# Kernel optimization log

Hardware: AMD Instinct MI355X
Metric: run time of the kernel (lower is better)

The kernel has to match this reference:

```python
import jax, jax.numpy as jnp
import numpy as np

LOW_THRESH, HIGH_THRESH = 0.1, 0.2   # kornia canny defaults
HYST_ITERS = 10                      # fixed-point hysteresis iterations (fixed for jit)


def _gaussian_kernel5(sigma=1.0):
    x = jnp.arange(5, dtype=jnp.float32) - 2.0
    g = jnp.exp(-0.5 * (x / sigma) ** 2)
    g = g / g.sum()
    return jnp.outer(g, g)  # [5,5]


def _conv2d(x, k):
    # x: [B,1,H,W]; k: [kh,kw]; reflect pad + VALID conv == SAME with reflect border
    kh, kw = k.shape
    xp = jnp.pad(x, ((0, 0), (0, 0), (kh // 2, kh // 2), (kw // 2, kw // 2)), mode="reflect")
    return jax.lax.conv_general_dilated(
        xp, k[None, None], (1, 1), "VALID",
        dimension_numbers=("NCHW", "OIHW", "NCHW"))


def _shift(x, dy, dx):
    # value of neighbor at (i+dy, j+dx), zero-padded border; x: [B,1,H,W]
    H, W = x.shape[2], x.shape[3]
    xp = jnp.pad(x, ((0, 0), (0, 0), (1, 1), (1, 1)))
    return xp[:, :, 1 + dy:1 + dy + H, 1 + dx:1 + dx + W]


def _canny_edges(img):
    # img: [B,3,H,W] in [0,1] -> binary edge map [B,1,H,W]
    gray = 0.299 * img[:, :1] + 0.587 * img[:, 1:2] + 0.114 * img[:, 2:3]
    blur = _conv2d(gray, _gaussian_kernel5())
    sobel_x = jnp.array([[-1., 0., 1.], [-2., 0., 2.], [-1., 0., 1.]], jnp.float32)
    gx = _conv2d(blur, sobel_x)
    gy = _conv2d(blur, sobel_x.T)
    mag = jnp.sqrt(gx * gx + gy * gy + 1e-12)
    ang = jnp.arctan2(gy, gx)

    # non-maximum suppression: quantize gradient direction to 4 bins (0/45/90/135 deg)
    b = jnp.mod(jnp.round(ang / (jnp.pi / 4.0)), 4).astype(jnp.int32)  # [B,1,H,W]
    n_pos = jnp.stack([_shift(mag, 0, 1), _shift(mag, 1, 1),
                       _shift(mag, 1, 0), _shift(mag, 1, -1)], axis=0)  # [4,B,1,H,W]
    n_neg = jnp.stack([_shift(mag, 0, -1), _shift(mag, -1, -1),
                       _shift(mag, -1, 0), _shift(mag, -1, 1)], axis=0)
    n1 = jnp.take_along_axis(n_pos, b[None], axis=0)[0]
    n2 = jnp.take_along_axis(n_neg, b[None], axis=0)[0]
    nms = jnp.where((mag >= n1) & (mag >= n2), mag, 0.0)

    # double threshold: strong=1.0, weak=0.5
    edges = jnp.where(nms >= HIGH_THRESH, 1.0,
                      jnp.where(nms >= LOW_THRESH, 0.5, 0.0))

    # hysteresis: weak pixels with a strong 8-neighbor become strong (iterated)
    def body(_, e):
        strong = (e == 1.0).astype(e.dtype)
        nb = jax.lax.reduce_window(strong, 0.0, jax.lax.max,
                                   (1, 1, 3, 3), (1, 1, 1, 1), "SAME")
        promoted = (e == 0.5) & (nb > 0.5)
        return jnp.where(promoted, 1.0, e)

    edges = jax.lax.fori_loop(0, HYST_ITERS, body, edges)
    return (edges == 1.0).astype(jnp.float32)


def setup_inputs() -> dict:
    key = jax.random.key(0)
    k1, k2 = jax.random.split(key)
    shape = (16, 3, 512, 512)
    return {"y_hat": jax.random.uniform(k1, shape, jnp.float32),
            "y": jax.random.uniform(k2, shape, jnp.float32)}


def reference(y_hat, y):
    y_hat_edges = _canny_edges(y_hat)
    y_edges = _canny_edges(y)
    return jnp.mean(jnp.abs(y_hat_edges - y_edges))  # F.l1_loss, mean reduction
```

## Files before the change

kernel.cpp:

```cpp
#include <hip/hip_runtime.h>
#include <math.h>

#define H 512
#define W 512
#define IMG (H*W)
#define NIMG 32
#define NSTRIP 10
#define SW 56
#define RB 32
#define NBAND 16
#define NHYST_BLK 1024

typedef unsigned long long u64;

__device__ __forceinline__ int reflect_idx(int i, int n) {
    if (i < 0) i = -i;
    if (i >= n) i = 2 * n - 2 - i;
    return i;
}

__device__ __forceinline__ float bperm_f(int addr, float v) {
    return __int_as_float(__builtin_amdgcn_ds_bpermute(addr, __float_as_int(v)));
}

#define S0c 0.05448868454964294f
#define S1c 0.35317871110251920f
#define S2c 0.94551131545035710f
#define S3c 1.29364257779496160f
#define A1c 0.05448868454964294f
#define A2c 0.24420134200323332f
#define A3c 0.34813126234460456f

__global__ __launch_bounds__(256, 5) void k_edges(const float* __restrict__ yhat,
                                                  const float* __restrict__ yy,
                                                  u64* __restrict__ strongP,
                                                  u64* __restrict__ weakP,
                                                  unsigned int* __restrict__ counters) {
    const int wid = blockIdx.x * 4 + (threadIdx.x >> 6);
    const int lane = threadIdx.x & 63;

    if (wid == 0 && lane == 0) { counters[0] = 0u; counters[1] = 0u; }

    const int n = wid / (NSTRIP * NBAND);
    const int rem = wid - n * (NSTRIP * NBAND);
    const int s = rem / NBAND;
    const int band = rem - s * NBAND;
    const int y0 = band * RB;
    const float* src = (n < 16) ? (yhat + (size_t)n * 3 * IMG)
                                : (yy + (size_t)(n - 16) * 3 * IMG);
    const float* __restrict__ srcR = src;
    const float* __restrict__ srcG = src + IMG;
    const float* __restrict__ srcB = src + 2 * IMG;

    const int c = s * SW - 4 + lane;
    const int cx = reflect_idx(c, W);
    const bool colok = ((unsigned)c < (unsigned)W);
    const u64 omask = (s == 9) ? 0xFFull : 0x00FFFFFFFFFFFFFFull;

    const int aM1 = ((lane - 1) << 2), aP1 = ((lane + 1) << 2);
    const int aM2 = ((lane - 2) << 2), aP2 = ((lane + 2) << 2);
    const int aM3 = ((lane - 3) << 2), aP3 = ((lane + 3) << 2);

    float hx[8], hy[8];
#pragma unroll
    for (int j = 0; j < 8; j++) { hx[j] = 0.f; hy[j] = 0.f; }

    const u64 outBase = ((size_t)n * NSTRIP + s) * H;

    float rA0, gA0, bA0, rA1, gA1, bA1;
    float rB0, gB0, bB0, rB1, gB1, bB1;

#define LOADP(S, kk)                                                            \
    {                                                                           \
        int ya = y0 - 4 + 2 * (kk), yb = ya + 1;                                \
        int ia = reflect_idx(ya, H), ib = reflect_idx(yb, H);                   \
        int voa = (ia << 9) + cx, vob = (ib << 9) + cx;                         \
        r##S##0 = srcR[voa]; g##S##0 = srcG[voa]; b##S##0 = srcB[voa];          \
        r##S##1 = srcR[vob]; g##S##1 = srcG[vob]; b##S##1 = srcB[vob];          \
    }

#define SHUF6(gv, t)                                                            \
    float t##m1 = bperm_f(aM1, gv), t##p1 = bperm_f(aP1, gv);                   \
    float t##m2 = bperm_f(aM2, gv), t##p2 = bperm_f(aP2, gv);                   \
    float t##m3 = bperm_f(aM3, gv), t##p3 = bperm_f(aP3, gv);

#define COMB(gv, t, P)                                                          \
    hx[(P) & 7] = A3c * (t##p1 - t##m1) + A2c * (t##p2 - t##m2)                 \
                + A1c * (t##p3 - t##m3);                                        \
    hy[(P) & 7] = S3c * (gv) + S2c * (t##p1 + t##m1) + S1c * (t##p2 + t##m2)    \
                + S0c * (t##p3 + t##m3);

#define MAG_AT(CP, mr, mv, mvL, mvR, dv)                                        \
    {                                                                           \
        float gx = S3c * hx[(CP) & 7]                                           \
                 + S2c * (hx[((CP) + 1) & 7] + hx[((CP) + 7) & 7])              \
                 + S1c * (hx[((CP) + 2) & 7] + hx[((CP) + 6) & 7])              \
                 + S0c * (hx[((CP) + 3) & 7] + hx[((CP) + 5) & 7]);             \
        float gy = A3c * (hy[((CP) + 1) & 7] - hy[((CP) + 7) & 7])              \
                 + A2c * (hy[((CP) + 2) & 7] - hy[((CP) + 6) & 7])              \
                 + A1c * (hy[((CP) + 3) & 7] - hy[((CP) + 5) & 7]);             \
        bool okm = colok && ((unsigned)(mr) < (unsigned)H);                     \
        mv = okm ? (gx * gx + gy * gy + 1e-12f) : 0.f;                          \
        mvL = bperm_f(aM1, mv);                                                 \
        mvR = bperm_f(aP1, mv);                                                 \
        float ax = fabsf(gx), ay = fabsf(gy);                                   \
        dv = (ay <= 0.4142135623730951f * ax) ? 0                               \
           : (ay >= 2.414213562373095f * ax) ? 2                                \
           : (((gx > 0.f) == (gy > 0.f)) ? 1 : 3);                              \
    }

#define GRAY0(S) (0.299f * r##S##0 + 0.587f * g##S##0 + 0.114f * b##S##0)
#define GRAY1(S) (0.299f * r##S##1 + 0.587f * g##S##1 + 0.114f * b##S##1)

    LOADP(A, 0);
    LOADP(B, 1);

#define PRIME(kk, S)                                                            \
    {                                                                           \
        float ga = GRAY0(S);                                                    \
        float gb = GRAY1(S);                                                    \
        LOADP(S, (kk) + 2);                                                     \
        SHUF6(ga, ta)                                                           \
        SHUF6(gb, tb)                                                           \
        COMB(ga, ta, 2 * (kk))                                                  \
        COMB(gb, tb, 2 * (kk) + 1)                                              \
    }
    PRIME(0, A)
    PRIME(1, B)
    PRIME(2, A)
#undef PRIME

    float mm1, mm1L, mm1R, m0, m0L, m0R;
    int dir0;
    {
        float ga = GRAY0(B);
        float gb = GRAY1(B);
        LOADP(B, 5);
        SHUF6(ga, ta)
        SHUF6(gb, tb)
        COMB(ga, ta, 6)
        int dtmp;
        MAG_AT(3, y0 - 1, mm1, mm1L, mm1R, dtmp);
        (void)dtmp;
        COMB(gb, tb, 7)
        MAG_AT(4, y0, m0, m0L, m0R, dir0);
    }

#define STEP(jj, k, S, DOPREF)                                                  \
    {                                                                           \
        float ga = GRAY0(S);                                                    \
        float gb = GRAY1(S);                                                    \
        if (DOPREF) LOADP(S, (k) + 2);                                          \
        SHUF6(ga, ta)                                                           \
        SHUF6(gb, tb)                                                           \
        float ma, maL, maR, mb, mbL, mbR;                                       \
        int da, db;                                                             \
        COMB(ga, ta, 2 * (jj))                                                  \
        MAG_AT((2 * (jj) + 5) & 7, y0 + 2 * (k) - 7, ma, maL, maR, da);         \
        COMB(gb, tb, 2 * (jj) + 1)                                              \
        MAG_AT((2 * (jj) + 6) & 7, y0 + 2 * (k) - 6, mb, mbL, mbR, db);         \
                                \
        float n1 = (dir0 == 0) ? m0R : (dir0 == 1) ? maR : (dir0 == 2) ? ma : maL; \
        float n2 = (dir0 == 0) ? m0L : (dir0 == 1) ? mm1L : (dir0 == 2) ? mm1 : mm1R; \
        bool ok0 = (m0 >= n1) && (m0 >= n2);                                    \
        u64 bs0 = __ballot(ok0 && (m0 >= 0.04f));                               \
        u64 bw0 = __ballot(ok0 && (m0 >= 0.01f));                               \
                                \
        float n3 = (da == 0) ? maR : (da == 1) ? mbR : (da == 2) ? mb : mbL;    \
        float n4 = (da == 0) ? maL : (da == 1) ? m0L : (da == 2) ? m0 : m0R;    \
        bool ok1 = (ma >= n3) && (ma >= n4);                                    \
        u64 bs1 = __ballot(ok1 && (ma >= 0.04f));                               \
        u64 bw1 = __ballot(ok1 && (ma >= 0.01f));                               \
        if (lane == 0) {                                                        \
            int t0 = y0 + 2 * (k) - 8;                                          \
            ulonglong2 vs, vw;                                                  \
            vs.x = (bs0 >> 4) & omask; vs.y = (bs1 >> 4) & omask;               \
            vw.x = (bw0 >> 4) & omask; vw.y = (bw1 >> 4) & omask;               \
            *(ulonglong2*)&strongP[outBase + t0] = vs;                          \
            *(ulonglong2*)&weakP[outBase + t0] = vw;                            \
        }                                                                       \
        mm1 = ma; mm1L = maL; mm1R = maR;                                       \
        m0 = mb; m0L = mbL; m0R = mbR;                                          \
        dir0 = db;                                                              \
    }

#pragma unroll 1
    for (int k4 = 4; k4 < 16; k4 += 4) {
        STEP(0, k4 + 0, A, true);
        STEP(1, k4 + 1, B, true);
        STEP(2, k4 + 2, A, true);
        STEP(3, k4 + 3, B, true);
    }
    STEP(0, 16, A, true);
    STEP(1, 17, B, true);
    STEP(2, 18, A, false);
    STEP(3, 19, B, false);

#undef STEP
#undef MAG_AT
#undef COMB
#undef SHUF6
#undef LOADP
#undef GRAY0
#undef GRAY1
}

__device__ __forceinline__ u64 ldw10(const u64* p, int img, int y, int q, bool ok) {
    return (ok && q >= 0 && q < NSTRIP) ? p[((size_t)img * NSTRIP + q) * H + y] : 0ULL;
}

__global__ __launch_bounds__(256) void k_hyst(const u64* __restrict__ strongP,
                                              const u64* __restrict__ weakP,
                                              unsigned int* __restrict__ counters,
                                              float* __restrict__ out) {
    __shared__ unsigned int part[4];
    const int wy = threadIdx.x >> 6;
    const int wave = blockIdx.x * 4 + wy;
    const int lane = threadIdx.x & 63;
    const int tile = wave & 255;
    const int pair = wave >> 8;
    const int tx0 = (tile & 15) * 32;
    const int ty0 = (tile >> 4) * 32;

    const int y = ty0 - 10 + lane;
    const bool rowok = (lane < 52) && (y >= 0) && (y < H);
    const int yc = rowok ? y : 0;

    const int x = tx0 - 10;
    const int q0 = (x < 0) ? -1 : (x / 56);
    const int r = x - 56 * q0;
    const int sh1 = 56 - r;
    const bool need3 = (r > 48);
    const int sh2 = 112 - r;

    const int imgA = pair, imgB = pair + 16;
    u64 sA, wA, sB, wB;
    {
        u64 w0, w1, w2;
        w0 = ldw10(strongP, imgA, yc, q0, rowok);
        w1 = ldw10(strongP, imgA, yc, q0 + 1, rowok);
        w2 = need3 ? ldw10(strongP, imgA, yc, q0 + 2, rowok) : 0ULL;
        sA = (w0 >> r) | (w1 << sh1) | (need3 ? (w2 << sh2) : 0ULL);
        w0 = ldw10(weakP, imgA, yc, q0, rowok);
        w1 = ldw10(weakP, imgA, yc, q0 + 1, rowok);
        w2 = need3 ? ldw10(weakP, imgA, yc, q0 + 2, rowok) : 0ULL;
        wA = (w0 >> r) | (w1 << sh1) | (need3 ? (w2 << sh2) : 0ULL);
        w0 = ldw10(strongP, imgB, yc, q0, rowok);
        w1 = ldw10(strongP, imgB, yc, q0 + 1, rowok);
        w2 = need3 ? ldw10(strongP, imgB, yc, q0 + 2, rowok) : 0ULL;
        sB = (w0 >> r) | (w1 << sh1) | (need3 ? (w2 << sh2) : 0ULL);
        w0 = ldw10(weakP, imgB, yc, q0, rowok);
        w1 = ldw10(weakP, imgB, yc, q0 + 1, rowok);
        w2 = need3 ? ldw10(weakP, imgB, yc, q0 + 2, rowok) : 0ULL;
        wB = (w0 >> r) | (w1 << sh1) | (need3 ? (w2 << sh2) : 0ULL);
    }

#pragma unroll
    for (int it = 0; it < 10; it++) {
        u64 up = __shfl_up(sA, 1), dn = __shfl_down(sA, 1);
        u64 t = up | sA | dn;
        sA |= (t | (t << 1) | (t >> 1)) & wA;
        up = __shfl_up(sB, 1); dn = __shfl_down(sB, 1);
        t = up | sB | dn;
        sB |= (t | (t << 1) | (t >> 1)) & wB;
    }

    unsigned int cgt = 0;
    if (lane >= 10 && lane < 42) {
        const u64 mask = ((1ULL << 42) - (1ULL << 10));
        cgt = (unsigned int)__popcll((sA ^ sB) & mask);
    }
#pragma unroll
    for (int off = 32; off > 0; off >>= 1) cgt += __shfl_down(cgt, off);
    if (lane == 0) part[wy] = cgt;
    __syncthreads();
    if (threadIdx.x == 0) {
        unsigned int tot = part[0] + part[1] + part[2] + part[3];
        atomicAdd(&counters[0], tot);
        __threadfence();
        unsigned int t = atomicAdd(&counters[1], 1u);
        if (t == NHYST_BLK - 1) {
            unsigned int total = atomicAdd(&counters[0], 0u);
            out[0] = (float)total * (1.0f / 4194304.0f);
        }
    }
}

extern "C" void kernel_launch(void* const* d_in, const int* in_sizes, int n_in,
                              void* d_out, int out_size, void* d_ws, size_t ws_size,
                              hipStream_t stream) {
    const float* yhat = (const float*)d_in[0];
    const float* yy = (const float*)d_in[1];

    u64* strongP = (u64*)d_ws;
    u64* weakP = strongP + (size_t)NIMG * NSTRIP * H;
    unsigned int* counters = (unsigned int*)(weakP + (size_t)NIMG * NSTRIP * H);

    k_edges<<<1280, 256, 0, stream>>>(yhat, yy, strongP, weakP, counters);

    k_hyst<<<1024, 256, 0, stream>>>(strongP, weakP, counters, (float*)d_out);
}
```

Baseline: 155.0 us.

## Software-pipeline gray/shuffle of next row pair; replace atomic reduction with final kernel

In the edge kernel, the gray conversion and lane shuffles for the next row pair are now issued at the end of each step, after the current gradient and magnitude work. This lets the ds_bpermute latency overlap with the non-max suppression and packing. The hysteresis kernel now writes per-block partial counts instead of using atomics with a last-block check, and a new single-block kernel sums them. This removes the atomic serialization and the counter reset, at the cost of an extra kernel launch.

```diff
diff --git a/kernel.cpp b/kernel.cpp
--- a/kernel.cpp
+++ b/kernel.cpp
@@ -9,7 +9,6 @@
 #define SW 56
 #define RB 32
 #define NBAND 16
-#define NHYST_BLK 1024
 
 typedef unsigned long long u64;
 
@@ -34,12 +33,9 @@
 __global__ __launch_bounds__(256, 5) void k_edges(const float* __restrict__ yhat,
                                                   const float* __restrict__ yy,
                                                   u64* __restrict__ strongP,
-                                                  u64* __restrict__ weakP,
-                                                  unsigned int* __restrict__ counters) {
+                                                  u64* __restrict__ weakP) {
     const int wid = blockIdx.x * 4 + (threadIdx.x >> 6);
     const int lane = threadIdx.x & 63;
-
-    if (wid == 0 && lane == 0) { counters[0] = 0u; counters[1] = 0u; }
 
     const int n = wid / (NSTRIP * NBAND);
     const int rem = wid - n * (NSTRIP * NBAND);
@@ -70,6 +66,10 @@
     float rA0, gA0, bA0, rA1, gA1, bA1;
     float rB0, gB0, bB0, rB1, gB1, bB1;
 
+    float sam1, sap1, sam2, sap2, sam3, sap3;
+    float sbm1, sbp1, sbm2, sbp2, sbm3, sbp3;
+    float gcur0, gcur1;
+
 #define LOADP(S, kk)                                                            \
     {                                                                           \
         int ya = y0 - 4 + 2 * (kk), yb = ya + 1;                                \
@@ -80,9 +80,9 @@
     }
 
 #define SHUF6(gv, t)                                                            \
-    float t##m1 = bperm_f(aM1, gv), t##p1 = bperm_f(aP1, gv);                   \
-    float t##m2 = bperm_f(aM2, gv), t##p2 = bperm_f(aP2, gv);                   \
-    float t##m3 = bperm_f(aM3, gv), t##p3 = bperm_f(aP3, gv);
+    t##m1 = bperm_f(aM1, gv); t##p1 = bperm_f(aP1, gv);                         \
+    t##m2 = bperm_f(aM2, gv); t##p2 = bperm_f(aP2, gv);                         \
+    t##m3 = bperm_f(aM3, gv); t##p3 = bperm_f(aP3, gv);
 
 #define COMB(gv, t, P)                                                          \
     hx[(P) & 7] = A3c * (t##p1 - t##m1) + A2c * (t##p2 - t##m2)                 \
@@ -120,10 +120,10 @@
         float ga = GRAY0(S);                                                    \
         float gb = GRAY1(S);                                                    \
         LOADP(S, (kk) + 2);                                                     \
-        SHUF6(ga, ta)                                                           \
-        SHUF6(gb, tb)                                                           \
-        COMB(ga, ta, 2 * (kk))                                                  \
-        COMB(gb, tb, 2 * (kk) + 1)                                              \
+        SHUF6(ga, sa)                                                           \
+        SHUF6(gb, sb)                                                           \
+        COMB(ga, sa, 2 * (kk))                                                  \
+        COMB(gb, sb, 2 * (kk) + 1)                                              \
     }
     PRIME(0, A)
     PRIME(1, B)
@@ -136,29 +136,36 @@
         float ga = GRAY0(B);
         float gb = GRAY1(B);
         LOADP(B, 5);
-        SHUF6(ga, ta)
-        SHUF6(gb, tb)
-        COMB(ga, ta, 6)
+        SHUF6(ga, sa)
+        SHUF6(gb, sb)
+        COMB(ga, sa, 6)
         int dtmp;
         MAG_AT(3, y0 - 1, mm1, mm1L, mm1R, dtmp);
         (void)dtmp;
-        COMB(gb, tb, 7)
+        COMB(gb, sb, 7)
         MAG_AT(4, y0, m0, m0L, m0R, dir0);
-    }
-
-#define STEP(jj, k, S, DOPREF)                                                  \
+        gcur0 = GRAY0(A);
+        gcur1 = GRAY1(A);
+        LOADP(A, 6);
+        SHUF6(gcur0, sa)
+        SHUF6(gcur1, sb)
+    }
+
+#define STEP(jj, k, SN, DOPREF, DONEXT)                                         \
     {                                                                           \
-        float ga = GRAY0(S);                                                    \
-        float gb = GRAY1(S);                                                    \
-        if (DOPREF) LOADP(S, (k) + 2);                                          \
-        SHUF6(ga, ta)                                                           \
-        SHUF6(gb, tb)                                                           \
         float ma, maL, maR, mb, mbL, mbR;                                       \
         int da, db;                                                             \
-        COMB(ga, ta, 2 * (jj))                                                  \
+        COMB(gcur0, sa, 2 * (jj))                                               \
         MAG_AT((2 * (jj) + 5) & 7, y0 + 2 * (k) - 7, ma, maL, maR, da);         \
-        COMB(gb, tb, 2 * (jj) + 1)                                              \
+        COMB(gcur1, sb, 2 * (jj) + 1)                                           \
         MAG_AT((2 * (jj) + 6) & 7, y0 + 2 * (k) - 6, mb, mbL, mbR, db);         \
+        if (DONEXT) {                                                           \
+            gcur0 = GRAY0(SN);                                                  \
+            gcur1 = GRAY1(SN);                                                  \
+            if (DOPREF) LOADP(SN, (k) + 3);                                     \
+            SHUF6(gcur0, sa)                                                    \
+            SHUF6(gcur1, sb)                                                    \
+        }                                                                       \
                                 \
         float n1 = (dir0 == 0) ? m0R : (dir0 == 1) ? maR : (dir0 == 2) ? ma : maL; \
         float n2 = (dir0 == 0) ? m0L : (dir0 == 1) ? mm1L : (dir0 == 2) ? mm1 : mm1R; \
@@ -186,15 +193,15 @@
 
 #pragma unroll 1
     for (int k4 = 4; k4 < 16; k4 += 4) {
-        STEP(0, k4 + 0, A, true);
-        STEP(1, k4 + 1, B, true);
-        STEP(2, k4 + 2, A, true);
-        STEP(3, k4 + 3, B, true);
-    }
-    STEP(0, 16, A, true);
-    STEP(1, 17, B, true);
-    STEP(2, 18, A, false);
-    STEP(3, 19, B, false);
+        STEP(0, k4 + 0, B, true, true);
+        STEP(1, k4 + 1, A, true, true);
+        STEP(2, k4 + 2, B, true, true);
+        STEP(3, k4 + 3, A, true, true);
+    }
+    STEP(0, 16, B, true, true);
+    STEP(1, 17, A, false, true);
+    STEP(2, 18, B, false, true);
+    STEP(3, 19, A, false, false);
 
 #undef STEP
 #undef MAG_AT
@@ -211,8 +218,7 @@
 
 __global__ __launch_bounds__(256) void k_hyst(const u64* __restrict__ strongP,
                                               const u64* __restrict__ weakP,
-                                              unsigned int* __restrict__ counters,
-                                              float* __restrict__ out) {
+                                              unsigned int* __restrict__ partials) {
     __shared__ unsigned int part[4];
     const int wy = threadIdx.x >> 6;
     const int wave = blockIdx.x * 4 + wy;
@@ -274,16 +280,23 @@
     for (int off = 32; off > 0; off >>= 1) cgt += __shfl_down(cgt, off);
     if (lane == 0) part[wy] = cgt;
     __syncthreads();
-    if (threadIdx.x == 0) {
-        unsigned int tot = part[0] + part[1] + part[2] + part[3];
-        atomicAdd(&counters[0], tot);
-        __threadfence();
-        unsigned int t = atomicAdd(&counters[1], 1u);
-        if (t == NHYST_BLK - 1) {
-            unsigned int total = atomicAdd(&counters[0], 0u);
-            out[0] = (float)total * (1.0f / 4194304.0f);
-        }
-    }
+    if (threadIdx.x == 0)
+        partials[blockIdx.x] = part[0] + part[1] + part[2] + part[3];
+}
+
+__global__ __launch_bounds__(256) void k_final(const unsigned int* __restrict__ partials,
+                                               float* __restrict__ out) {
+    __shared__ unsigned int part[4];
+    unsigned int c = 0;
+    for (int i = threadIdx.x; i < 1024; i += 256) c += partials[i];
+#pragma unroll
+    for (int off = 32; off > 0; off >>= 1) c += __shfl_down(c, off);
+    const int lane = threadIdx.x & 63;
+    const int wy = threadIdx.x >> 6;
+    if (lane == 0) part[wy] = c;
+    __syncthreads();
+    if (threadIdx.x == 0)
+        out[0] = (float)(part[0] + part[1] + part[2] + part[3]) * (1.0f / 4194304.0f);
 }
 
 extern "C" void kernel_launch(void* const* d_in, const int* in_sizes, int n_in,
@@ -294,9 +307,10 @@
 
     u64* strongP = (u64*)d_ws;
     u64* weakP = strongP + (size_t)NIMG * NSTRIP * H;
-    unsigned int* counters = (unsigned int*)(weakP + (size_t)NIMG * NSTRIP * H);
-
-    k_edges<<<1280, 256, 0, stream>>>(yhat, yy, strongP, weakP, counters);
-
-    k_hyst<<<1024, 256, 0, stream>>>(strongP, weakP, counters, (float*)d_out);
-}
+    unsigned int* partials = (unsigned int*)(weakP + (size_t)NIMG * NSTRIP * H);
+
+    k_edges<<<1280, 256, 0, stream>>>(yhat, yy, strongP, weakP);
+
+    k_hyst<<<1024, 256, 0, stream>>>(strongP, weakP, partials);
+    k_final<<<1, 256, 0, stream>>>(partials, (float*)d_out);
+}
```

New measurement: 230.2 us. +48.5%, slower.
